# Optimization experiments

Hardware: AMD Instinct MI355X
Metric: run time of the kernel (lower is better)

## Reference

```python
import jax, jax.numpy as jnp
import numpy as np


def setup_inputs() -> dict:
    key = jax.random.key(0)
    k1, k2 = jax.random.split(key)
    B, L, D, R = 32, 512, 1024, 128
    batch = jax.random.normal(k1, (B, L, D), dtype=jnp.float32)
    # nn.init.uniform_(proj, -0.05, 0.05)
    proj = jax.random.uniform(k2, (D, R), dtype=jnp.float32, minval=-0.05, maxval=0.05)
    return {"batch": batch, "proj": proj}


def reference(batch, proj):
    # transformed: (B, L, R)
    t = jnp.matmul(batch, proj)
    # Squared L2 all-pairs distance via ||a||^2 + ||b||^2 - 2 a.b
    # (same math as sum((t_i - t_j)^2, -1), avoids the O(B*L*L*R) intermediate)
    sq_norms = jnp.sum(t * t, axis=-1)                      # (B, L)
    cross = jnp.einsum("bir,bjr->bij", t, t)               # (B, L, L)
    d = sq_norms[:, :, None] + sq_norms[:, None, :] - 2.0 * cross
    return jnp.maximum(d, 0.0)  # clamp tiny negative numerical noise
```

## Files before the change

kernel.cpp:

```cpp
#include <hip/hip_runtime.h>
#include <hip/hip_bf16.h>


typedef __attribute__((ext_vector_type(8))) short bf16x8;
typedef __attribute__((ext_vector_type(4))) float f32x4;

typedef __attribute__((address_space(3))) unsigned lds_u;
typedef __attribute__((address_space(1))) const unsigned gbl_u;

__device__ __forceinline__ void async16(void* lds, const void* g) {
    __builtin_amdgcn_global_load_lds((gbl_u*)(unsigned long long)g,
                                     (lds_u*)(unsigned)(unsigned long long)lds,
                                     16, 0, 0);
}

__device__ __forceinline__ unsigned short f2bf(float f) {
    unsigned u = __float_as_uint(f);
    unsigned r = (u + 0x7fffu + ((u >> 16) & 1u)) >> 16;
    return (unsigned short)r;
}
__device__ __forceinline__ float bf2f(unsigned short h) {
    return __uint_as_float(((unsigned)h) << 16);
}
__device__ __forceinline__ bf16x8 pack8(float4 x, float4 y) {
    bf16x8 r;
    r[0] = (short)f2bf(x.x); r[1] = (short)f2bf(x.y);
    r[2] = (short)f2bf(x.z); r[3] = (short)f2bf(x.w);
    r[4] = (short)f2bf(y.x); r[5] = (short)f2bf(y.y);
    r[6] = (short)f2bf(y.z); r[7] = (short)f2bf(y.w);
    return r;
}

__global__ __launch_bounds__(256) void transpose_proj(const float* __restrict__ proj,
                                                      unsigned short* __restrict__ projT) {
    __shared__ unsigned short TsT[128][40];
    const int k0 = blockIdx.x * 32;
    const int t = threadIdx.x;
    const int kl = t >> 3;
    const int seg = t & 7;
    const float* src = proj + (k0 + kl) * 128 + seg * 16;
#pragma unroll
    for (int i = 0; i < 4; ++i) {
        float4 v = *(const float4*)(src + 4 * i);
        int c = seg * 16 + 4 * i;
        TsT[c + 0][kl] = f2bf(v.x);
        TsT[c + 1][kl] = f2bf(v.y);
        TsT[c + 2][kl] = f2bf(v.z);
        TsT[c + 3][kl] = f2bf(v.w);
    }
    __syncthreads();
    const int r = t >> 1, h = t & 1;
#pragma unroll
    for (int i = 0; i < 2; ++i) {
        *(uint4*)(projT + r * 1024 + k0 + h * 16 + 8 * i) =
            *(const uint4*)&TsT[r][h * 16 + 8 * i];
    }
}

__global__ __launch_bounds__(256) void gemm_t(const float* __restrict__ batch,
                                              const unsigned short* __restrict__ projT,
                                              unsigned short* __restrict__ tOut,
                                              float* __restrict__ sqn) {
    __shared__ unsigned char Ls[2][8 * 1024];
    __shared__ float sqpart[2][2][16];

    const int t = threadIdx.x;
    const int wave = t >> 6, lane = t & 63;
    const int wm = wave >> 1, wn = wave & 1;
    const int quad = lane >> 4, l15 = lane & 15;
    const int m0 = blockIdx.x * 32;

    f32x4 acc[4] = {};

    const float* aSrc = batch + (m0 + (wave >> 1) * 16 + l15) * 1024
                      + (wave & 1) * 32 + quad * 8;
    const unsigned short* bSrc[4][2];
#pragma unroll
    for (int fn = 0; fn < 4; ++fn)
#pragma unroll
        for (int h = 0; h < 2; ++h)
            bSrc[fn][h] = projT + (wn * 64 + fn * 16 + l15) * 1024 + h * 32 + quad * 8;

    auto stageA = [&](int buf, int kk) {
        unsigned char* base = &Ls[buf][0];
        async16(base + (wave * 2 + 0) * 1024 + lane * 16, aSrc + kk);
        async16(base + (wave * 2 + 1) * 1024 + lane * 16, aSrc + kk + 4);
    };

    stageA(0, 0);
#pragma unroll
    for (int s = 0; s < 16; ++s) {
        const int kk = s * 64;
        bf16x8 breg[4][2];
#pragma unroll
        for (int fn = 0; fn < 4; ++fn)
#pragma unroll
            for (int h = 0; h < 2; ++h)
                breg[fn][h] = *(const bf16x8*)(bSrc[fn][h] + kk);
        __syncthreads();
        if (s < 15) stageA((s + 1) & 1, kk + 64);
        const unsigned char* base = &Ls[s & 1][0];
        bf16x8 af[2];
#pragma unroll
        for (int h = 0; h < 2; ++h) {
            float4 f0 = *(const float4*)(base + ((wm * 2 + h) * 2 + 0) * 1024 + lane * 16);
            float4 f1 = *(const float4*)(base + ((wm * 2 + h) * 2 + 1) * 1024 + lane * 16);
            af[h] = pack8(f0, f1);
        }
#pragma unroll
        for (int h = 0; h < 2; ++h)
#pragma unroll
            for (int fn = 0; fn < 4; ++fn)
                acc[fn] = __builtin_amdgcn_mfma_f32_16x16x32_bf16(af[h], breg[fn][h], acc[fn], 0, 0, 0);
    }

    float p[4] = {0.f, 0.f, 0.f, 0.f};
#pragma unroll
    for (int fn = 0; fn < 4; ++fn) {
        int col = wn * 64 + fn * 16 + l15;
#pragma unroll
        for (int reg = 0; reg < 4; ++reg) {
            int row = m0 + wm * 16 + quad * 4 + reg;
            unsigned short hb = f2bf(acc[fn][reg]);
            tOut[row * 128 + col] = hb;
            float fv = bf2f(hb);
            p[reg] += fv * fv;
        }
    }
#pragma unroll
    for (int off = 1; off < 16; off <<= 1) {
#pragma unroll
        for (int reg = 0; reg < 4; ++reg) p[reg] += __shfl_xor(p[reg], off);
    }
    if (l15 == 0) {
#pragma unroll
        for (int reg = 0; reg < 4; ++reg) sqpart[wm][wn][quad * 4 + reg] = p[reg];
    }
    __syncthreads();
    if (t < 32) {
        int wmi = t >> 4, ridx = t & 15;
        sqn[m0 + wmi * 16 + ridx] = sqpart[wmi][0][ridx] + sqpart[wmi][1][ridx];
    }
}

__global__ __launch_bounds__(256) void dist_k(const unsigned short* __restrict__ tMat,
                                              const float* __restrict__ sqn,
                                              float* __restrict__ out) {
    __shared__ unsigned char Ls[64 * 1024];

    const int bx = blockIdx.x;
    const int b = bx & 31, tile = bx >> 5;
    const int it = tile >> 2, jt = tile & 3;
    const int i0 = it * 128, j0 = jt * 128;
    const int t = threadIdx.x;
    const int wave = t >> 6, lane = t & 63;
    const int quad = lane >> 4, l15 = lane & 15;

    const unsigned short* aS = tMat + (b * 512 + j0 + wave * 32 + l15) * 128 + quad * 8;
    const unsigned short* bS = tMat + (b * 512 + i0 + l15) * 128 + quad * 8;

#pragma unroll
    for (int c = 0; c < 4; ++c) {
        int fm = c >> 1, ksi = c & 1;
        async16(&Ls[(wave * 8 + fm * 4 + ksi) * 1024 + lane * 16],
                aS + fm * 16 * 128 + ksi * 32);
    }
#pragma unroll
    for (int c = 0; c < 4; ++c) {
        int idx = wave * 4 + c, fn = idx >> 1, ksi = idx & 1;
        async16(&Ls[32768 + (fn * 4 + ksi) * 1024 + lane * 16],
                bS + fn * 16 * 128 + ksi * 32);
    }

    const float* sqb = sqn + b * 512;
    float sqj_[2][4], sqi_[8];
#pragma unroll
    for (int fm = 0; fm < 2; ++fm)
#pragma unroll
        for (int reg = 0; reg < 4; ++reg)
            sqj_[fm][reg] = sqb[j0 + wave * 32 + fm * 16 + quad * 4 + reg];
#pragma unroll
    for (int fn = 0; fn < 8; ++fn)
        sqi_[fn] = sqb[i0 + fn * 16 + l15];

    __syncthreads();

#pragma unroll
    for (int c = 0; c < 4; ++c) {
        int fm = c >> 1, ksi = 2 + (c & 1);
        async16(&Ls[(wave * 8 + fm * 4 + ksi) * 1024 + lane * 16],
                aS + fm * 16 * 128 + ksi * 32);
    }
#pragma unroll
    for (int c = 0; c < 4; ++c) {
        int idx = wave * 4 + c, fn = idx >> 1, ksi = 2 + (idx & 1);
        async16(&Ls[32768 + (fn * 4 + ksi) * 1024 + lane * 16],
                bS + fn * 16 * 128 + ksi * 32);
    }

    f32x4 acc[2][8] = {};
#pragma unroll
    for (int ksi = 0; ksi < 2; ++ksi) {
        bf16x8 af[2];
#pragma unroll
        for (int fm = 0; fm < 2; ++fm)
            af[fm] = *(const bf16x8*)&Ls[(wave * 8 + fm * 4 + ksi) * 1024 + lane * 16];
#pragma unroll
        for (int fn = 0; fn < 8; ++fn) {
            bf16x8 bfr = *(const bf16x8*)&Ls[32768 + (fn * 4 + ksi) * 1024 + lane * 16];
#pragma unroll
            for (int fm = 0; fm < 2; ++fm)
                acc[fm][fn] = __builtin_amdgcn_mfma_f32_16x16x32_bf16(af[fm], bfr, acc[fm][fn], 0, 0, 0);
        }
    }

    __syncthreads();

#pragma unroll
    for (int ksi = 2; ksi < 4; ++ksi) {
        bf16x8 af[2];
#pragma unroll
        for (int fm = 0; fm < 2; ++fm)
            af[fm] = *(const bf16x8*)&Ls[(wave * 8 + fm * 4 + ksi) * 1024 + lane * 16];
#pragma unroll
        for (int fn = 0; fn < 8; ++fn) {
            bf16x8 bfr = *(const bf16x8*)&Ls[32768 + (fn * 4 + ksi) * 1024 + lane * 16];
#pragma unroll
            for (int fm = 0; fm < 2; ++fm)
                acc[fm][fn] = __builtin_amdgcn_mfma_f32_16x16x32_bf16(af[fm], bfr, acc[fm][fn], 0, 0, 0);
        }
    }

    float* obase = out + (size_t)b * 512 * 512;
#pragma unroll
    for (int fn = 0; fn < 8; ++fn) {
        const int i = i0 + fn * 16 + l15;
        float* orow = obase + (size_t)i * 512 + j0;
        const float si = sqi_[fn];
#pragma unroll
        for (int fm = 0; fm < 2; ++fm) {
            float4 v;
            v.x = fmaxf(si + sqj_[fm][0] - 2.0f * acc[fm][fn][0], 0.0f);
            v.y = fmaxf(si + sqj_[fm][1] - 2.0f * acc[fm][fn][1], 0.0f);
            v.z = fmaxf(si + sqj_[fm][2] - 2.0f * acc[fm][fn][2], 0.0f);
            v.w = fmaxf(si + sqj_[fm][3] - 2.0f * acc[fm][fn][3], 0.0f);
            *(float4*)(orow + wave * 32 + fm * 16 + quad * 4) = v;
        }
    }
}

extern "C" void kernel_launch(void* const* d_in, const int* in_sizes, int n_in,
                              void* d_out, int out_size, void* d_ws, size_t ws_size,
                              hipStream_t stream) {
    (void)in_sizes; (void)n_in; (void)out_size; (void)ws_size;
    const float* batch = (const float*)d_in[0];
    const float* proj  = (const float*)d_in[1];
    float* out = (float*)d_out;

    unsigned short* projT = (unsigned short*)d_ws;
    unsigned short* tMat  = projT + 128 * 1024;
    float* sqn = (float*)(tMat + 16384 * 128);

    hipLaunchKernelGGL(transpose_proj, dim3(32),  dim3(256), 0, stream, proj, projT);
    hipLaunchKernelGGL(gemm_t,         dim3(512), dim3(256), 0, stream, batch, projT, tMat, sqn);
    hipLaunchKernelGGL(dist_k,         dim3(512), dim3(256), 0, stream, tMat, sqn, out);
}
```

Baseline: 137.5 us.

## Pre-convert batch to bf16 in separate kernel and restage gemm A tiles

Adds a standalone kernel that converts the fp32 batch to bf16 in workspace. The projection GEMM then stages bf16 A rows into LDS in two large half-K chunks, with no per-step fp32-to-bf16 packing. The aim is to remove conversion ALU work and fp32 LDS traffic from the GEMM inner loop. In exchange it adds an extra full write and re-read of the batch through HBM, and a much larger LDS footprint per block, which may reduce occupancy.

```diff
diff --git a/kernel.cpp b/kernel.cpp
--- a/kernel.cpp
+++ b/kernel.cpp
@@ -29,6 +29,19 @@
     r[4] = (short)f2bf(y.x); r[5] = (short)f2bf(y.y);
     r[6] = (short)f2bf(y.z); r[7] = (short)f2bf(y.w);
     return r;
+}
+
+__global__ __launch_bounds__(256) void convert_batch(const float* __restrict__ in,
+                                                     unsigned short* __restrict__ outB) {
+    size_t g = (size_t)(blockIdx.x * 256 + threadIdx.x) * 8;
+    const size_t stride = (size_t)2048 * 256 * 8;
+#pragma unroll
+    for (int i = 0; i < 4; ++i) {
+        size_t idx = g + (size_t)i * stride;
+        float4 a = *(const float4*)(in + idx);
+        float4 b = *(const float4*)(in + idx + 4);
+        *(bf16x8*)(outB + idx) = pack8(a, b);
+    }
 }
 
 __global__ __launch_bounds__(256) void transpose_proj(const float* __restrict__ proj,
@@ -57,11 +70,11 @@
     }
 }
 
-__global__ __launch_bounds__(256) void gemm_t(const float* __restrict__ batch,
+__global__ __launch_bounds__(256) void gemm_t(const unsigned short* __restrict__ batchB,
                                               const unsigned short* __restrict__ projT,
                                               unsigned short* __restrict__ tOut,
                                               float* __restrict__ sqn) {
-    __shared__ unsigned char Ls[2][8 * 1024];
+    __shared__ unsigned char Ls[2][32 * 1024];
     __shared__ float sqpart[2][2][16];
 
     const int t = threadIdx.x;
@@ -72,46 +85,32 @@
 
     f32x4 acc[4] = {};
 
-    const float* aSrc = batch + (m0 + (wave >> 1) * 16 + l15) * 1024
-                      + (wave & 1) * 32 + quad * 8;
-    const unsigned short* bSrc[4][2];
-#pragma unroll
-    for (int fn = 0; fn < 4; ++fn)
-#pragma unroll
-        for (int h = 0; h < 2; ++h)
-            bSrc[fn][h] = projT + (wn * 64 + fn * 16 + l15) * 1024 + h * 32 + quad * 8;
-
-    auto stageA = [&](int buf, int kk) {
-        unsigned char* base = &Ls[buf][0];
-        async16(base + (wave * 2 + 0) * 1024 + lane * 16, aSrc + kk);
-        async16(base + (wave * 2 + 1) * 1024 + lane * 16, aSrc + kk + 4);
+    auto stage = [&](int buf, int s) {
+#pragma unroll
+        for (int c = 0; c < 8; ++c) {
+            int row = wave * 8 + c;
+            async16(&Ls[buf][row * 1024 + lane * 16],
+                    batchB + (size_t)(m0 + row) * 1024 + s * 512 + lane * 8);
+        }
     };
 
-    stageA(0, 0);
-#pragma unroll
-    for (int s = 0; s < 16; ++s) {
-        const int kk = s * 64;
-        bf16x8 breg[4][2];
-#pragma unroll
-        for (int fn = 0; fn < 4; ++fn)
-#pragma unroll
-            for (int h = 0; h < 2; ++h)
-                breg[fn][h] = *(const bf16x8*)(bSrc[fn][h] + kk);
+    stage(0, 0);
+#pragma unroll
+    for (int s = 0; s < 2; ++s) {
         __syncthreads();
-        if (s < 15) stageA((s + 1) & 1, kk + 64);
-        const unsigned char* base = &Ls[s & 1][0];
-        bf16x8 af[2];
-#pragma unroll
-        for (int h = 0; h < 2; ++h) {
-            float4 f0 = *(const float4*)(base + ((wm * 2 + h) * 2 + 0) * 1024 + lane * 16);
-            float4 f1 = *(const float4*)(base + ((wm * 2 + h) * 2 + 1) * 1024 + lane * 16);
-            af[h] = pack8(f0, f1);
-        }
-#pragma unroll
-        for (int h = 0; h < 2; ++h)
-#pragma unroll
-            for (int fn = 0; fn < 4; ++fn)
-                acc[fn] = __builtin_amdgcn_mfma_f32_16x16x32_bf16(af[h], breg[fn][h], acc[fn], 0, 0, 0);
+        if (s == 0) stage(1, 1);
+        const unsigned char* Ab = &Ls[s][0];
+#pragma unroll
+        for (int k = 0; k < 16; ++k) {
+            bf16x8 af = *(const bf16x8*)(Ab + (wm * 16 + l15) * 1024 + k * 64 + quad * 16);
+            const int kg = s * 512 + k * 32;
+#pragma unroll
+            for (int fn = 0; fn < 4; ++fn) {
+                bf16x8 bfr = *(const bf16x8*)(projT + (wn * 64 + fn * 16 + l15) * 1024
+                                              + kg + quad * 8);
+                acc[fn] = __builtin_amdgcn_mfma_f32_16x16x32_bf16(af, bfr, acc[fn], 0, 0, 0);
+            }
+        }
     }
 
     float p[4] = {0.f, 0.f, 0.f, 0.f};
@@ -257,11 +256,13 @@
     const float* proj  = (const float*)d_in[1];
     float* out = (float*)d_out;
 
-    unsigned short* projT = (unsigned short*)d_ws;
-    unsigned short* tMat  = projT + 128 * 1024;
-    float* sqn = (float*)(tMat + 16384 * 128);
-
-    hipLaunchKernelGGL(transpose_proj, dim3(32),  dim3(256), 0, stream, proj, projT);
-    hipLaunchKernelGGL(gemm_t,         dim3(512), dim3(256), 0, stream, batch, projT, tMat, sqn);
-    hipLaunchKernelGGL(dist_k,         dim3(512), dim3(256), 0, stream, tMat, sqn, out);
-}
+    unsigned short* batchB = (unsigned short*)d_ws;
+    unsigned short* projT  = batchB + (size_t)16384 * 1024;
+    unsigned short* tMat   = projT + 128 * 1024;
+    float* sqn = (float*)(tMat + (size_t)16384 * 128);
+
+    hipLaunchKernelGGL(convert_batch,  dim3(2048), dim3(256), 0, stream, batch, batchB);
+    hipLaunchKernelGGL(transpose_proj, dim3(32),   dim3(256), 0, stream, proj, projT);
+    hipLaunchKernelGGL(gemm_t,         dim3(512),  dim3(256), 0, stream, batchB, projT, tMat, sqn);
+    hipLaunchKernelGGL(dist_k,         dim3(512),  dim3(256), 0, stream, tMat, sqn, out);
+}
```

Measured after the change: 149.4 us. +8.6%, slower.

## Stage projT B tiles through LDS with async loads alongside A

Applied to the files above, without the earlier changes.

The projection GEMM kernel previously loaded B fragments straight from global memory into registers each k-step. It now copies both the A tile and the B tile into double-buffered LDS with async global-to-LDS loads, and reorganises the A layout to suit. The goal is to overlap B loads with compute and cut redundant global traffic. In exchange, LDS use per block rises from 16KB to 48KB, which may lower occupancy, and the row-major B reads from LDS may hit bank conflicts.

```diff
diff --git a/kernel.cpp b/kernel.cpp
--- a/kernel.cpp
+++ b/kernel.cpp
@@ -61,7 +61,7 @@
                                               const unsigned short* __restrict__ projT,
                                               unsigned short* __restrict__ tOut,
                                               float* __restrict__ sqn) {
-    __shared__ unsigned char Ls[2][8 * 1024];
+    __shared__ unsigned char Ls[2][24 * 1024];
     __shared__ float sqpart[2][2][16];
 
     const int t = threadIdx.x;
@@ -72,46 +72,51 @@
 
     f32x4 acc[4] = {};
 
-    const float* aSrc = batch + (m0 + (wave >> 1) * 16 + l15) * 1024
-                      + (wave & 1) * 32 + quad * 8;
-    const unsigned short* bSrc[4][2];
-#pragma unroll
-    for (int fn = 0; fn < 4; ++fn)
-#pragma unroll
-        for (int h = 0; h < 2; ++h)
-            bSrc[fn][h] = projT + (wn * 64 + fn * 16 + l15) * 1024 + h * 32 + quad * 8;
-
-    auto stageA = [&](int buf, int kk) {
+    const float* aSrc[2];
+#pragma unroll
+    for (int c = 0; c < 2; ++c) {
+        int ca = wave * 2 + c;
+        aSrc[c] = batch + (size_t)(m0 + ca * 4 + (lane >> 4)) * 1024 + (lane & 15) * 4;
+    }
+    const unsigned short* bSrc[4];
+#pragma unroll
+    for (int c = 0; c < 4; ++c) {
+        int cb = wave * 4 + c;
+        bSrc[c] = projT + (size_t)(cb * 8 + (lane >> 3)) * 1024 + (lane & 7) * 8;
+    }
+
+    auto stage = [&](int buf, int kk) {
         unsigned char* base = &Ls[buf][0];
-        async16(base + (wave * 2 + 0) * 1024 + lane * 16, aSrc + kk);
-        async16(base + (wave * 2 + 1) * 1024 + lane * 16, aSrc + kk + 4);
+#pragma unroll
+        for (int c = 0; c < 2; ++c)
+            async16(base + (wave * 2 + c) * 1024 + lane * 16, aSrc[c] + kk);
+#pragma unroll
+        for (int c = 0; c < 4; ++c)
+            async16(base + 8192 + (wave * 4 + c) * 1024 + lane * 16, bSrc[c] + kk);
     };
 
-    stageA(0, 0);
+    stage(0, 0);
 #pragma unroll
     for (int s = 0; s < 16; ++s) {
-        const int kk = s * 64;
-        bf16x8 breg[4][2];
-#pragma unroll
-        for (int fn = 0; fn < 4; ++fn)
-#pragma unroll
-            for (int h = 0; h < 2; ++h)
-                breg[fn][h] = *(const bf16x8*)(bSrc[fn][h] + kk);
         __syncthreads();
-        if (s < 15) stageA((s + 1) & 1, kk + 64);
+        if (s < 15) stage((s + 1) & 1, (s + 1) * 64);
         const unsigned char* base = &Ls[s & 1][0];
         bf16x8 af[2];
 #pragma unroll
         for (int h = 0; h < 2; ++h) {
-            float4 f0 = *(const float4*)(base + ((wm * 2 + h) * 2 + 0) * 1024 + lane * 16);
-            float4 f1 = *(const float4*)(base + ((wm * 2 + h) * 2 + 1) * 1024 + lane * 16);
+            const unsigned char* ap = base + (wm * 16 + l15) * 256 + h * 128 + quad * 32;
+            float4 f0 = *(const float4*)(ap);
+            float4 f1 = *(const float4*)(ap + 16);
             af[h] = pack8(f0, f1);
         }
 #pragma unroll
         for (int h = 0; h < 2; ++h)
 #pragma unroll
-            for (int fn = 0; fn < 4; ++fn)
-                acc[fn] = __builtin_amdgcn_mfma_f32_16x16x32_bf16(af[h], breg[fn][h], acc[fn], 0, 0, 0);
+            for (int fn = 0; fn < 4; ++fn) {
+                bf16x8 bfr = *(const bf16x8*)(base + 8192 + (wn * 64 + fn * 16 + l15) * 128
+                                              + h * 64 + quad * 16);
+                acc[fn] = __builtin_amdgcn_mfma_f32_16x16x32_bf16(af[h], bfr, acc[fn], 0, 0, 0);
+            }
     }
 
     float p[4] = {0.f, 0.f, 0.f, 0.f};
@@ -259,7 +264,7 @@
 
     unsigned short* projT = (unsigned short*)d_ws;
     unsigned short* tMat  = projT + 128 * 1024;
-    float* sqn = (float*)(tMat + 16384 * 128);
+    float* sqn = (float*)(tMat + (size_t)16384 * 128);
 
     hipLaunchKernelGGL(transpose_proj, dim3(32),  dim3(256), 0, stream, proj, projT);
     hipLaunchKernelGGL(gemm_t,         dim3(512), dim3(256), 0, stream, batch, projT, tMat, sqn);
```

Measured after the change: 125.4 us. 8.8% less time.
